# Optimization experiments

Hardware: AMD Instinct MI355X
Metric: run time of the kernel (lower is better)

## Reference

```python
import jax, jax.numpy as jnp
import numpy as np

N = 50000      # nodes
E = 600000     # edges
IN = 128       # input_dim
HID = 128      # hidden_dim
OUT = 128      # output_dim
H = 4          # heads
D = OUT // H   # head dim
R = 4          # rel_num
L = 2          # n_layer
M = 10000      # len(idx)
EPS = 1e-5


def setup_inputs() -> dict:
    key = jax.random.key(0)
    ks = jax.random.split(key, 16)
    f = jax.random.normal
    inp = {
        "x": f(ks[0], (N, IN), jnp.float32),
        "proj_w": f(ks[1], (IN, HID), jnp.float32) / np.sqrt(IN).astype(np.float32),
        "proj_b": jnp.zeros((HID,), jnp.float32),
        "bn_gamma": jnp.ones((HID,), jnp.float32),
        "bn_beta": jnp.zeros((HID,), jnp.float32),
        # per-layer HGTConv params (stacked on leading L axis; layer0 in=HID, layer1 in=OUT, equal here)
        "q_w": f(ks[2], (L, HID, OUT), jnp.float32) / np.sqrt(HID).astype(np.float32),
        "q_b": jnp.zeros((L, OUT), jnp.float32),
        "k_w": f(ks[3], (L, HID, OUT), jnp.float32) / np.sqrt(HID).astype(np.float32),
        "k_b": jnp.zeros((L, OUT), jnp.float32),
        "v_w": f(ks[4], (L, HID, OUT), jnp.float32) / np.sqrt(HID).astype(np.float32),
        "v_b": jnp.zeros((L, OUT), jnp.float32),
        "a_w": f(ks[5], (L, OUT, OUT), jnp.float32) / np.sqrt(OUT).astype(np.float32),
        "a_b": jnp.zeros((L, OUT), jnp.float32),
        "skip": jnp.ones((L,), jnp.float32),
        "a_rel": f(ks[6], (L, R, H, D, D), jnp.float32) / np.sqrt(D).astype(np.float32),
        "m_rel": f(ks[7], (L, R, H, D, D), jnp.float32) / np.sqrt(D).astype(np.float32),
        "p_rel": jnp.ones((L, R, H), jnp.float32),
        "edge_index": jax.random.randint(ks[8], (2, E), 0, N, dtype=jnp.int32),
        "edge_type": jax.random.randint(ks[9], (E,), 0, R, dtype=jnp.int32),
        "idx": jax.random.randint(ks[10], (M,), 0, N, dtype=jnp.int32),
    }
    return inp


def _hgt_forward(x, proj_w, proj_b, bn_gamma, bn_beta, q_w, q_b, k_w, k_b, v_w, v_b,
                 a_w, a_b, skip, a_rel, m_rel, p_rel, edge_index, edge_type, idx):
    # proj + BatchNorm1d (training-mode batch statistics, biased variance)
    h = x @ proj_w + proj_b
    mu = h.mean(axis=0)
    var = jnp.mean((h - mu) ** 2, axis=0)
    h = (h - mu) * jax.lax.rsqrt(var + EPS) * bn_gamma + bn_beta

    src, dst = edge_index[0], edge_index[1]          # message from src(j) to dst(i)
    seg = dst * R + edge_type                        # per-(dst, relation) softmax segments
    scale = np.float32(1.0 / np.sqrt(D))

    for l in range(L):
        q = (h @ q_w[l] + q_b[l]).reshape(N, H, D)
        k = (h @ k_w[l] + k_b[l]).reshape(N, H, D)
        v = (h @ v_w[l] + v_b[l]).reshape(N, H, D)
        # relation-specific key/value transforms for every node/relation: [N,R,H,D]
        k_all = jnp.einsum('nhd,rhde->nrhe', k, a_rel[l])
        v_all = jnp.einsum('nhd,rhde->nrhe', v, m_rel[l])
        k_e = k_all[src, edge_type]                  # [E,H,D]
        v_e = v_all[src, edge_type]                  # [E,H,D]
        score = jnp.sum(q[dst] * k_e, axis=-1) * p_rel[l][edge_type] * scale  # [E,H]
        # per-relation segment softmax over incoming edges of each dst node
        smax = jax.ops.segment_max(score, seg, num_segments=N * R)
        e = jnp.exp(score - smax[seg])
        denom = jax.ops.segment_sum(e, seg, num_segments=N * R)
        alpha = e / denom[seg]                        # [E,H]
        out = jax.ops.segment_sum(alpha[..., None] * v_e, dst, num_segments=N)
        out = out.reshape(N, OUT)
        out = jax.nn.gelu(out, approximate=False) @ a_w[l] + a_b[l]
        b = jax.nn.sigmoid(skip[l])                   # learned skip gate
        h = b * out + (1.0 - b) * h                   # dims match -> residual mix
    return h[idx]


def reference(x, proj_w, proj_b, bn_gamma, bn_beta, q_w, q_b, k_w, k_b, v_w, v_b,
              a_w, a_b, skip, a_rel, m_rel, p_rel, edge_index, edge_type, idx):
    return _hgt_forward(x, proj_w, proj_b, bn_gamma, bn_beta, q_w, q_b, k_w, k_b,
                        v_w, v_b, a_w, a_b, skip, a_rel, m_rel, p_rel,
                        edge_index, edge_type, idx)
```

## Files before the change

kernel.cpp:

```cpp
#include <hip/hip_runtime.h>
#include <math.h>

#define NN 50000
#define EE 600000
#define MOUT 10000
#define DEGCAP 384
#define NT4 (NN * 4)

typedef short bf16x8 __attribute__((ext_vector_type(8)));
typedef float f32x4 __attribute__((ext_vector_type(4)));

__device__ __forceinline__ unsigned short f2bf(float x) {
    unsigned int u = __float_as_uint(x);
    u = (u + 0x7FFFu + ((u >> 16) & 1u)) >> 16;
    return (unsigned short)u;
}
__device__ __forceinline__ float bf2f(unsigned int b) {
    return __uint_as_float(b << 16);
}
__device__ __forceinline__ uint4 pack8bf(float4 a, float4 b) {
    uint4 r;
    r.x = (unsigned int)f2bf(a.x) | ((unsigned int)f2bf(a.y) << 16);
    r.y = (unsigned int)f2bf(a.z) | ((unsigned int)f2bf(a.w) << 16);
    r.z = (unsigned int)f2bf(b.x) | ((unsigned int)f2bf(b.y) << 16);
    r.w = (unsigned int)f2bf(b.z) | ((unsigned int)f2bf(b.w) << 16);
    return r;
}

__global__ __launch_bounds__(256) void prep_kernel(
    const float* __restrict__ proj_w, const float* __restrict__ a_w,
    const float* __restrict__ q_w, const float* __restrict__ q_b,
    const float* __restrict__ a_rel,
    const float* __restrict__ k_w, const float* __restrict__ k_b,
    const float* __restrict__ v_w, const float* __restrict__ v_b,
    const float* __restrict__ m_rel, const float* __restrict__ p_rel,
    unsigned short* __restrict__ wt_pa, unsigned short* __restrict__ qkvw,
    float* __restrict__ fbias, unsigned short* __restrict__ msg_wt,
    int* __restrict__ cnt, float* __restrict__ stats)
{
    const int b = blockIdx.x, t = threadIdx.x;
    if (b < 192) {
        int wi = b >> 6;
        int flat = (b & 63) * 256 + t;
        int n = flat >> 7, c = flat & 127;
        const float* src = (wi == 0) ? proj_w : (wi == 1) ? a_w : a_w + 16384;
        wt_pa[(size_t)wi * 16384 + n * 128 + c] = f2bf(src[c * 128 + n]);
    } else if (b < 960) {
        int q = b - 192;
        int l = q >= 384 ? 1 : 0;
        int flat = (q - l * 384) * 256 + t;
        int nrow = flat >> 7, c = flat & 127;
        unsigned short* wt = qkvw + (size_t)l * 98304;
        float* fb = fbias + l * 768;
        if (nrow < 512) {
            int r = nrow >> 7, hh = (nrow >> 5) & 3, d = nrow & 31;
            float prl = p_rel[l * 16 + r * 4 + hh] * 0.17677669529663687f;
            const float* qwc = q_w + (size_t)l * 16384 + c * 128 + hh * 32;
            const float* ar  = a_rel + (size_t)(l * 4 + r) * 4096 + hh * 1024 + d * 32;
            float s = 0.f;
            #pragma unroll 8
            for (int e = 0; e < 32; ++e) s += qwc[e] * ar[e];
            wt[(size_t)nrow * 128 + c] = f2bf(s * prl);
            if (c == 0) {
                const float* qb = q_b + l * 128 + hh * 32;
                float bb = 0.f;
                #pragma unroll 8
                for (int e = 0; e < 32; ++e) bb += qb[e] * ar[e];
                fb[nrow] = bb * prl;
            }
        } else {
            int j = nrow - 512;
            int tt = j >> 3, s = j & 7;
            int col = 4 * tt + (s & 3);
            const float* w  = (s < 4) ? k_w : v_w;
            const float* bb = (s < 4) ? k_b : v_b;
            wt[(size_t)nrow * 128 + c] = f2bf(w[(size_t)l * 16384 + c * 128 + col]);
            if (c == 0) fb[nrow] = bb[l * 128 + col];
        }
    } else if (b < 1088) {
        int q = b - 960;
        int l = q >= 64 ? 1 : 0;
        int flat = (q - l * 64) * 256 + t;
        int r = flat >> 12, rem = flat & 4095;
        int n = rem >> 5, d = rem & 31;
        float val = m_rel[(size_t)(l * 4 + r) * 4096 + (n >> 5) * 1024 + d * 32 + (n & 31)];
        msg_wt[(size_t)l * 16384 + r * 4096 + n * 32 + d] = f2bf(val);
    } else {
        int i = (b - 1088) * 256 + t;
        if (i < NT4) cnt[i] = 0;
        if (i < 256) stats[i] = 0.f;
    }
}

__global__ __launch_bounds__(256) void hist_kernel(const int* __restrict__ ei,
    const int* __restrict__ et, int* __restrict__ cnt, int E)
{
    int e = blockIdx.x * 256 + threadIdx.x;
    if (e < E) atomicAdd(&cnt[ei[E + e] * 4 + et[e]], 1);
}

__global__ __launch_bounds__(256) void scan_block_kernel(const int* __restrict__ cnt,
    int* __restrict__ excl, int* __restrict__ bsum, int n)
{
    __shared__ int tmp[256];
    int i = blockIdx.x * 256 + threadIdx.x;
    int v = (i < n) ? cnt[i] : 0;
    tmp[threadIdx.x] = v;
    __syncthreads();
    for (int ofs = 1; ofs < 256; ofs <<= 1) {
        int t = (threadIdx.x >= ofs) ? tmp[threadIdx.x - ofs] : 0;
        __syncthreads();
        tmp[threadIdx.x] += t;
        __syncthreads();
    }
    if (i < n) excl[i] = tmp[threadIdx.x] - v;
    if (threadIdx.x == 255) bsum[blockIdx.x] = tmp[255];
}

__global__ __launch_bounds__(256) void scan_add_kernel(int* __restrict__ excl,
    const int* __restrict__ bsum, int* __restrict__ fill,
    int* __restrict__ maskz, int n, int total)
{
    __shared__ int red[256];
    const int b = blockIdx.x;
    int partial = 0;
    for (int j = threadIdx.x; j < b; j += 256) partial += bsum[j];
    red[threadIdx.x] = partial;
    __syncthreads();
    for (int ofs = 128; ofs > 0; ofs >>= 1) {
        if (threadIdx.x < ofs) red[threadIdx.x] += red[threadIdx.x + ofs];
        __syncthreads();
    }
    int prefix = red[0];
    int i = b * 256 + threadIdx.x;
    if (i < n) {
        int o = excl[i] + prefix;
        excl[i] = o;
        fill[i] = o;
    }
    if (i < 12500) maskz[i] = 0;
    if (b == 0 && threadIdx.x == 0) excl[n] = total;
}

__global__ __launch_bounds__(256) void scatter_kernel(const int* __restrict__ ei,
    const int* __restrict__ et, int* __restrict__ fill, int* __restrict__ pack,
    const int* __restrict__ idxp, unsigned char* __restrict__ mask, int Mo, int E)
{
    int e = blockIdx.x * 256 + threadIdx.x;
    if (e >= E) return;
    int seg = ei[E + e] * 4 + et[e];
    int p = atomicAdd(&fill[seg], 1);
    pack[p] = ei[e];
    if (e < Mo) mask[idxp[e]] = 1;
}

__global__ __launch_bounds__(256) void projstats_kernel(
    const float* __restrict__ X, const unsigned short* __restrict__ Wt,
    const float* __restrict__ bias, unsigned short* __restrict__ Cb,
    float* __restrict__ stats, int M)
{
    __shared__ unsigned short As[128 * 40];
    __shared__ unsigned short Bs[128 * 40];
    const int t = threadIdx.x;
    const int wave = t >> 6, lane = t & 63;
    const int quad = lane >> 4, l16 = lane & 15;
    const int row0 = blockIdx.x * 128;
    const int wr = (wave & 1) * 64, wc = (wave >> 1) * 64;
    const int sr = t >> 1, sc = (t & 1) * 16;
    const int grow = row0 + sr;

    f32x4 acc[4][4];
    #pragma unroll
    for (int i = 0; i < 4; ++i)
        #pragma unroll
        for (int j = 0; j < 4; ++j)
            acc[i][j] = (f32x4){0.f, 0.f, 0.f, 0.f};

    uint4 av0 = make_uint4(0,0,0,0), av1 = av0, bv0, bv1;
    if (grow < M) {
        const float4* ap = (const float4*)(X + (size_t)grow * 128 + sc);
        av0 = pack8bf(ap[0], ap[1]);
        av1 = pack8bf(ap[2], ap[3]);
    }
    {
        const uint4* bp = (const uint4*)(Wt + (size_t)sr * 128 + sc);
        bv0 = bp[0]; bv1 = bp[1];
    }
    for (int it = 0; it < 4; ++it) {
        __syncthreads();
        *(uint4*)(As + sr * 40 + sc)     = av0;
        *(uint4*)(As + sr * 40 + sc + 8) = av1;
        *(uint4*)(Bs + sr * 40 + sc)     = bv0;
        *(uint4*)(Bs + sr * 40 + sc + 8) = bv1;
        __syncthreads();
        if (it + 1 < 4) {
            int kb = (it + 1) * 32;
            if (grow < M) {
                const float4* ap = (const float4*)(X + (size_t)grow * 128 + kb + sc);
                av0 = pack8bf(ap[0], ap[1]);
                av1 = pack8bf(ap[2], ap[3]);
            }
            const uint4* bp = (const uint4*)(Wt + (size_t)sr * 128 + kb + sc);
            bv0 = bp[0]; bv1 = bp[1];
        }
        bf16x8 af[4], bfr[4];
        #pragma unroll
        for (int f = 0; f < 4; ++f) {
            af[f]  = *(const bf16x8*)(As + (wr + f * 16 + l16) * 40 + quad * 8);
            bfr[f] = *(const bf16x8*)(Bs + (wc + f * 16 + l16) * 40 + quad * 8);
        }
        #pragma unroll
        for (int fr = 0; fr < 4; ++fr)
            #pragma unroll
            for (int fc = 0; fc < 4; ++fc)
                acc[fr][fc] = __builtin_amdgcn_mfma_f32_16x16x32_bf16(
                    af[fr], bfr[fc], acc[fr][fc], 0, 0, 0);
    }

    #pragma unroll
    for (int fc = 0; fc < 4; ++fc) {
        const int col = wc + fc * 16 + l16;
        const float bv = bias[col];
        float s = 0.f, s2 = 0.f;
        #pragma unroll
        for (int fr = 0; fr < 4; ++fr)
            #pragma unroll
            for (int reg = 0; reg < 4; ++reg) {
                int row = row0 + wr + fr * 16 + quad * 4 + reg;
                float val = acc[fr][fc][reg] + bv;
                if (row < M) {
                    Cb[(size_t)row * 128 + col] = f2bf(val);
                    s += val; s2 += val * val;
                }
            }
        s  += __shfl_xor(s, 16);  s  += __shfl_xor(s, 32);
        s2 += __shfl_xor(s2, 16); s2 += __shfl_xor(s2, 32);
        if (quad == 0) {
            atomicAdd(&stats[col], s);
            atomicAdd(&stats[128 + col], s2);
        }
    }
}

__global__ __launch_bounds__(256) void bnqkv_kernel(
    const unsigned short* __restrict__ hb, const float* __restrict__ stats,
    const float* __restrict__ gamma, const float* __restrict__ beta,
    const unsigned short* __restrict__ qkvw, const float* __restrict__ fbias,
    unsigned short* __restrict__ hn, unsigned short* __restrict__ qkv, int M)
{
    __shared__ unsigned short hS[128 * 136];
    __shared__ unsigned short Bs[128 * 40];
    __shared__ float mulS[128], addS[128];
    const int t = threadIdx.x;
    const int row0 = blockIdx.x * 128;
    const int ch0 = blockIdx.y * 2;
    if (t < 128) {
        float invN = 1.f / 50000.f;
        float mu = stats[t] * invN;
        float var = stats[128 + t] * invN - mu * mu;
        float ml = rsqrtf(var + 1e-5f) * gamma[t];
        mulS[t] = ml;
        addS[t] = beta[t] - mu * ml;
    }
    __syncthreads();
    #pragma unroll
    for (int u = 0; u < 8; ++u) {
        int li = t + u * 256;
        int row = li >> 4, c0 = (li & 15) * 8;
        uint4 pk = make_uint4(0, 0, 0, 0);
        if (row0 + row < M)
            pk = ((const uint4*)(hb + (size_t)(row0 + row) * 128))[li & 15];
        unsigned int w[4] = {pk.x, pk.y, pk.z, pk.w};
        uint4 o;
        unsigned int ov[4];
        #pragma unroll
        for (int g = 0; g < 4; ++g) {
            int c = c0 + g * 2;
            float a0 = bf2f(w[g] & 0xFFFFu) * mulS[c]     + addS[c];
            float a1 = bf2f(w[g] >> 16)     * mulS[c + 1] + addS[c + 1];
            ov[g] = (unsigned int)f2bf(a0) | ((unsigned int)f2bf(a1) << 16);
        }
        o.x = ov[0]; o.y = ov[1]; o.z = ov[2]; o.w = ov[3];
        *(uint4*)(hS + row * 136 + c0) = o;
        if (blockIdx.y == 0 && row0 + row < M)
            ((uint4*)(hn + (size_t)(row0 + row) * 128))[li & 15] = o;
    }
    __syncthreads();

    const int wave = t >> 6, lane = t & 63;
    const int quad = lane >> 4, l16 = lane & 15;
    const int wr = (wave & 1) * 64, wcl = (wave >> 1) * 64;
    const int sr = t >> 1, scc = (t & 1) * 16;

    uint4 pv0, pv1;
    {
        const uint4* bp = (const uint4*)(qkvw + (size_t)(ch0 * 128 + sr) * 128 + scc);
        pv0 = bp[0]; pv1 = bp[1];
    }
    for (int ch = ch0; ch < ch0 + 2; ++ch) {
        f32x4 acc[4][4];
        #pragma unroll
        for (int i = 0; i < 4; ++i)
            #pragma unroll
            for (int j = 0; j < 4; ++j)
                acc[i][j] = (f32x4){0.f, 0.f, 0.f, 0.f};
        for (int it = 0; it < 4; ++it) {
            __syncthreads();
            *(uint4*)(Bs + sr * 40 + scc)     = pv0;
            *(uint4*)(Bs + sr * 40 + scc + 8) = pv1;
            __syncthreads();
            int nit = it + 1, nch = ch;
            if (nit == 4) { nit = 0; ++nch; }
            if (nch < ch0 + 2) {
                const uint4* bp = (const uint4*)(qkvw + (size_t)(nch * 128 + sr) * 128 + nit * 32 + scc);
                pv0 = bp[0]; pv1 = bp[1];
            }
            bf16x8 af[4], bfr[4];
            #pragma unroll
            for (int f = 0; f < 4; ++f) {
                af[f]  = *(const bf16x8*)(hS + (wr + f * 16 + l16) * 136 + it * 32 + quad * 8);
                bfr[f] = *(const bf16x8*)(Bs + (wcl + f * 16 + l16) * 40 + quad * 8);
            }
            #pragma unroll
            for (int fr = 0; fr < 4; ++fr)
                #pragma unroll
                for (int fc = 0; fc < 4; ++fc)
                    acc[fr][fc] = __builtin_amdgcn_mfma_f32_16x16x32_bf16(
                        af[fr], bfr[fc], acc[fr][fc], 0, 0, 0);
        }
        float b4[4];
        #pragma unroll
        for (int fc = 0; fc < 4; ++fc)
            b4[fc] = fbias[ch * 128 + wcl + fc * 16 + l16];
        #pragma unroll
        for (int fr = 0; fr < 4; ++fr)
            #pragma unroll
            for (int reg = 0; reg < 4; ++reg) {
                int row = row0 + wr + fr * 16 + quad * 4 + reg;
                if (row >= M) continue;
                #pragma unroll
                for (int fc = 0; fc < 4; ++fc) {
                    int col = ch * 128 + wcl + fc * 16 + l16;
                    qkv[(size_t)row * 768 + col] = f2bf(acc[fr][fc][reg] + b4[fc]);
                }
            }
    }
}

__global__ __launch_bounds__(256) void agg_fused_kernel(
    const unsigned short* __restrict__ qkv,
    const unsigned short* __restrict__ qbuf, int qpitch,
    const int* __restrict__ off4, const int* __restrict__ pack,
    const int* __restrict__ rowmap, unsigned short* __restrict__ aggb, int count)
{
    __shared__ int spack[4][DEGCAP];
    const int wv = threadIdx.x >> 6;
    const int lane = threadIdx.x & 63;
    const int l32 = lane & 31;
    const int hi = lane >> 5;
    const int unit = blockIdx.x * 4 + wv;
    if (unit >= count) return;
    const int node = rowmap ? __builtin_amdgcn_readfirstlane(rowmap[unit]) : unit;

    const uint2* qrow = (const uint2*)(qbuf + (size_t)unit * qpitch);
    uint2 quv[4];
    #pragma unroll
    for (int r = 0; r < 4; ++r) quv[r] = qrow[r * 32 + l32];

    int off_r[5];
    #pragma unroll
    for (int i = 0; i < 5; ++i)
        off_r[i] = __builtin_amdgcn_readfirstlane(off4[node * 4 + i]);
    const int beg = off_r[0];
    const int deg = off_r[4] - beg;
    const bool cached = deg <= DEGCAP;

    if (cached) {
        for (int i = lane; i < deg; i += 64) spack[wv][i] = pack[beg + i];
        asm volatile("s_waitcnt vmcnt(0) lgkmcnt(0)" ::: "memory");
    }

    uint2 outw[4];
    #pragma unroll
    for (int r = 0; r < 4; ++r) {
        float q0 = bf2f(quv[r].x & 0xFFFFu), q1 = bf2f(quv[r].x >> 16);
        float q2 = bf2f(quv[r].y & 0xFFFFu), q3 = bf2f(quv[r].y >> 16);
        float den = 0.f, a0 = 0.f, a1 = 0.f, a2 = 0.f, a3 = 0.f;

        if (cached) {
            const int rb = off_r[r] - beg, re = off_r[r + 1] - beg;
            for (int i = rb; i < re; i += 4) {
                int i0 = i + hi;      if (i0 >= re) i0 = re - 1;
                int i1 = i + 2 + hi;  if (i1 >= re) i1 = re - 1;
                int s0 = spack[wv][i0], s1 = spack[wv][i1];
                uint4 kv0 = *(const uint4*)(qkv + (size_t)s0 * 768 + 512 + l32 * 8);
                uint4 kv1 = *(const uint4*)(qkv + (size_t)s1 * 768 + 512 + l32 * 8);
                {
                    float p = q0 * bf2f(kv0.x & 0xFFFFu) + q1 * bf2f(kv0.x >> 16)
                            + q2 * bf2f(kv0.y & 0xFFFFu) + q3 * bf2f(kv0.y >> 16);
                    p += __shfl_xor(p, 1); p += __shfl_xor(p, 2); p += __shfl_xor(p, 4);
                    float e = __expf(fminf(fmaxf(p, -80.f), 80.f));
                    if (i + hi >= re) e = 0.f;
                    den += e;
                    a0 += e * bf2f(kv0.z & 0xFFFFu); a1 += e * bf2f(kv0.z >> 16);
                    a2 += e * bf2f(kv0.w & 0xFFFFu); a3 += e * bf2f(kv0.w >> 16);
                }
                {
                    float p = q0 * bf2f(kv1.x & 0xFFFFu) + q1 * bf2f(kv1.x >> 16)
                            + q2 * bf2f(kv1.y & 0xFFFFu) + q3 * bf2f(kv1.y >> 16);
                    p += __shfl_xor(p, 1); p += __shfl_xor(p, 2); p += __shfl_xor(p, 4);
                    float e = __expf(fminf(fmaxf(p, -80.f), 80.f));
                    if (i + 2 + hi >= re) e = 0.f;
                    den += e;
                    a0 += e * bf2f(kv1.z & 0xFFFFu); a1 += e * bf2f(kv1.z >> 16);
                    a2 += e * bf2f(kv1.w & 0xFFFFu); a3 += e * bf2f(kv1.w >> 16);
                }
            }
        } else {
            const int pe_end = off_r[r + 1];
            for (int pp = off_r[r]; pp < pe_end; pp += 2) {
                int pe = pp + hi; if (pe >= pe_end) pe = pe_end - 1;
                int src = pack[pe];
                uint4 kv = *(const uint4*)(qkv + (size_t)src * 768 + 512 + l32 * 8);
                float p = q0 * bf2f(kv.x & 0xFFFFu) + q1 * bf2f(kv.x >> 16)
                        + q2 * bf2f(kv.y & 0xFFFFu) + q3 * bf2f(kv.y >> 16);
                p += __shfl_xor(p, 1); p += __shfl_xor(p, 2); p += __shfl_xor(p, 4);
                float e = __expf(fminf(fmaxf(p, -80.f), 80.f));
                if (pp + hi >= pe_end) e = 0.f;
                den += e;
                a0 += e * bf2f(kv.z & 0xFFFFu); a1 += e * bf2f(kv.z >> 16);
                a2 += e * bf2f(kv.w & 0xFFFFu); a3 += e * bf2f(kv.w >> 16);
            }
        }
        den += __shfl_xor(den, 32);
        a0  += __shfl_xor(a0, 32);
        a1  += __shfl_xor(a1, 32);
        a2  += __shfl_xor(a2, 32);
        a3  += __shfl_xor(a3, 32);
        float inv = den > 0.f ? 1.f / den : 0.f;
        outw[r].x = (unsigned int)f2bf(a0 * inv) | ((unsigned int)f2bf(a1 * inv) << 16);
        outw[r].y = (unsigned int)f2bf(a2 * inv) | ((unsigned int)f2bf(a3 * inv) << 16);
    }
    if (hi == 0) {
        uint2* op = (uint2*)(aggb + (size_t)unit * 512);
        #pragma unroll
        for (int r = 0; r < 4; ++r) op[r * 32 + l32] = outw[r];
    }
}

__global__ __launch_bounds__(256) void mlpqkv_kernel(
    const unsigned short* __restrict__ A, const unsigned short* __restrict__ W3c,
    const unsigned short* __restrict__ AWt, const float* __restrict__ a_bias,
    const float* __restrict__ skipv, const unsigned short* __restrict__ hres,
    const unsigned short* __restrict__ qkvw1, const float* __restrict__ fbias1,
    const unsigned char* __restrict__ mask,
    unsigned short* __restrict__ h1, unsigned short* __restrict__ qkv, int M)
{
    __shared__ unsigned short Bs[128 * 40];
    __shared__ unsigned short msgS[64 * 136];
    const int t = threadIdx.x;
    const int wave = t >> 6, lane = t & 63;
    const int quad = lane >> 4, l16 = lane & 15;
    const int row0 = blockIdx.x * 64;
    const int wcl = wave * 32;
    const int sr = t >> 1, scc = (t & 1) * 16;
    const int sr4 = t >> 2, sc4 = (t & 3) * 32;
    const int grow = row0 + sr4;
    const bool rvalid = grow < M;

    f32x4 acc[4][2];
    #pragma unroll
    for (int i = 0; i < 4; ++i)
        #pragma unroll
        for (int j = 0; j < 2; ++j)
            acc[i][j] = (f32x4){0.f, 0.f, 0.f, 0.f};

    uint4 av[4];
    #pragma unroll
    for (int j = 0; j < 4; ++j) av[j] = make_uint4(0, 0, 0, 0);
    if (rvalid) {
        const uint4* ap = (const uint4*)(A + (size_t)grow * 512 + sc4);
        #pragma unroll
        for (int j = 0; j < 4; ++j) av[j] = ap[j];
    }
    uint4 bw0, bw1;
    {
        const uint4* bp = (const uint4*)(W3c + sr * 32 + scc);
        bw0 = bp[0]; bw1 = bp[1];
    }
    for (int it = 0; it < 4; ++it) {
        __syncthreads();
        #pragma unroll
        for (int j = 0; j < 4; ++j)
            *(uint4*)(msgS + sr4 * 136 + sc4 + j * 8) = av[j];
        *(uint4*)(Bs + sr * 40 + scc)     = bw0;
        *(uint4*)(Bs + sr * 40 + scc + 8) = bw1;
        __syncthreads();
        if (it + 1 < 4) {
            if (rvalid) {
                const uint4* ap = (const uint4*)(A + (size_t)grow * 512 + (it + 1) * 128 + sc4);
                #pragma unroll
                for (int j = 0; j < 4; ++j) av[j] = ap[j];
            }
            const uint4* bp = (const uint4*)(W3c + (it + 1) * 4096 + sr * 32 + scc);
            bw0 = bp[0]; bw1 = bp[1];
        }
        bf16x8 af[4], bfr[2];
        #pragma unroll
        for (int f = 0; f < 4; ++f)
            af[f] = *(const bf16x8*)(msgS + (f * 16 + l16) * 136 + wave * 32 + quad * 8);
        #pragma unroll
        for (int f = 0; f < 2; ++f)
            bfr[f] = *(const bf16x8*)(Bs + (wcl + f * 16 + l16) * 40 + quad * 8);
        #pragma unroll
        for (int fr = 0; fr < 4; ++fr)
            #pragma unroll
            for (int fc = 0; fc < 2; ++fc)
                acc[fr][fc] = __builtin_amdgcn_mfma_f32_16x16x32_bf16(
                    af[fr], bfr[fc], acc[fr][fc], 0, 0, 0);
    }
    __syncthreads();

    #pragma unroll
    for (int fr = 0; fr < 4; ++fr)
        #pragma unroll
        for (int reg = 0; reg < 4; ++reg) {
            int rl = fr * 16 + quad * 4 + reg;
            #pragma unroll
            for (int fc = 0; fc < 2; ++fc) {
                int col = wcl + fc * 16 + l16;
                float v = acc[fr][fc][reg];
                float gl = 0.5f * v * (1.f + erff(v * 0.70710678118654752f));
                msgS[rl * 136 + col] = f2bf(gl);
            }
        }

    f32x4 acc2[4][2];
    #pragma unroll
    for (int i = 0; i < 4; ++i)
        #pragma unroll
        for (int j = 0; j < 2; ++j)
            acc2[i][j] = (f32x4){0.f, 0.f, 0.f, 0.f};
    uint4 pv0, pv1;
    {
        const uint4* bp = (const uint4*)(AWt + (size_t)sr * 128 + scc);
        pv0 = bp[0]; pv1 = bp[1];
    }
    for (int it = 0; it < 4; ++it) {
        __syncthreads();
        *(uint4*)(Bs + sr * 40 + scc)     = pv0;
        *(uint4*)(Bs + sr * 40 + scc + 8) = pv1;
        __syncthreads();
        if (it + 1 < 4) {
            const uint4* bp = (const uint4*)(AWt + (size_t)sr * 128 + (it + 1) * 32 + scc);
            pv0 = bp[0]; pv1 = bp[1];
        } else {
            const uint4* bp = (const uint4*)(qkvw1 + (size_t)(4 * 128 + sr) * 128 + scc);
            pv0 = bp[0]; pv1 = bp[1];
        }
        bf16x8 af[4], bfr[2];
        #pragma unroll
        for (int f = 0; f < 4; ++f)
            af[f] = *(const bf16x8*)(msgS + (f * 16 + l16) * 136 + it * 32 + quad * 8);
        #pragma unroll
        for (int f = 0; f < 2; ++f)
            bfr[f] = *(const bf16x8*)(Bs + (wcl + f * 16 + l16) * 40 + quad * 8);
        #pragma unroll
        for (int fr = 0; fr < 4; ++fr)
            #pragma unroll
            for (int fc = 0; fc < 2; ++fc)
                acc2[fr][fc] = __builtin_amdgcn_mfma_f32_16x16x32_bf16(
                    af[fr], bfr[fc], acc2[fr][fc], 0, 0, 0);
    }

    const float gate = 1.f / (1.f + __expf(-skipv[0]));
    __syncthreads();
    #pragma unroll
    for (int fr = 0; fr < 4; ++fr)
        #pragma unroll
        for (int reg = 0; reg < 4; ++reg) {
            int rl = fr * 16 + quad * 4 + reg;
            int row = row0 + rl;
            const bool rv = row < M;
            const bool mw = rv && mask[row];
            #pragma unroll
            for (int fc = 0; fc < 2; ++fc) {
                int col = wcl + fc * 16 + l16;
                float val = acc2[fr][fc][reg] + a_bias[col];
                float nv = val;
                if (rv) {
                    unsigned int hu = hres[(size_t)row * 128 + col];
                    nv = gate * val + (1.f - gate) * bf2f(hu);
                    if (mw) h1[(size_t)row * 128 + col] = f2bf(nv);
                }
                msgS[rl * 136 + col] = f2bf(nv);
            }
        }

    for (int ch = 4; ch < 6; ++ch) {
        f32x4 acc3[4][2];
        #pragma unroll
        for (int i = 0; i < 4; ++i)
            #pragma unroll
            for (int j = 0; j < 2; ++j)
                acc3[i][j] = (f32x4){0.f, 0.f, 0.f, 0.f};
        for (int it = 0; it < 4; ++it) {
            __syncthreads();
            *(uint4*)(Bs + sr * 40 + scc)     = pv0;
            *(uint4*)(Bs + sr * 40 + scc + 8) = pv1;
            __syncthreads();
            int nit = it + 1, nch = ch;
            if (nit == 4) { nit = 0; ++nch; }
            if (nch < 6) {
                const uint4* bp = (const uint4*)(qkvw1 + (size_t)(nch * 128 + sr) * 128 + nit * 32 + scc);
                pv0 = bp[0]; pv1 = bp[1];
            }
            bf16x8 af[4], bfr[2];
            #pragma unroll
            for (int f = 0; f < 4; ++f)
                af[f] = *(const bf16x8*)(msgS + (f * 16 + l16) * 136 + it * 32 + quad * 8);
            #pragma unroll
            for (int f = 0; f < 2; ++f)
                bfr[f] = *(const bf16x8*)(Bs + (wcl + f * 16 + l16) * 40 + quad * 8);
            #pragma unroll
            for (int fr = 0; fr < 4; ++fr)
                #pragma unroll
                for (int fc = 0; fc < 2; ++fc)
                    acc3[fr][fc] = __builtin_amdgcn_mfma_f32_16x16x32_bf16(
                        af[fr], bfr[fc], acc3[fr][fc], 0, 0, 0);
        }
        float b2[2];
        #pragma unroll
        for (int fc = 0; fc < 2; ++fc)
            b2[fc] = fbias1[ch * 128 + wcl + fc * 16 + l16];
        #pragma unroll
        for (int fr = 0; fr < 4; ++fr)
            #pragma unroll
            for (int reg = 0; reg < 4; ++reg) {
                int row = row0 + fr * 16 + quad * 4 + reg;
                if (row >= M) continue;
                #pragma unroll
                for (int fc = 0; fc < 2; ++fc) {
                    int col = ch * 128 + wcl + fc * 16 + l16;
                    qkv[(size_t)row * 768 + col] = f2bf(acc3[fr][fc][reg] + b2[fc]);
                }
            }
    }
}

__global__ __launch_bounds__(256) void q1_kernel(
    const unsigned short* __restrict__ h1, const int* __restrict__ idxp,
    const unsigned short* __restrict__ qkvw1, const float* __restrict__ fbias1,
    unsigned short* __restrict__ q1, int M)
{
    __shared__ unsigned short hS[128 * 136];
    __shared__ unsigned short Bs[128 * 40];
    const int t = threadIdx.x;
    const int row0 = blockIdx.x * 128;
    const int ch = blockIdx.y;
    #pragma unroll
    for (int u = 0; u < 8; ++u) {
        int li = t + u * 256;
        int row = li >> 4, c = li & 15;
        uint4 pk = make_uint4(0, 0, 0, 0);
        if (row0 + row < M) {
            int node = idxp[row0 + row];
            pk = ((const uint4*)(h1 + (size_t)node * 128))[c];
        }
        *(uint4*)(hS + row * 136 + c * 8) = pk;
    }
    __syncthreads();

    const int wave = t >> 6, lane = t & 63;
    const int quad = lane >> 4, l16 = lane & 15;
    const int wr = (wave & 1) * 64, wcl = (wave >> 1) * 64;
    const int sr = t >> 1, scc = (t & 1) * 16;
    uint4 pv0, pv1;
    {
        const uint4* bp = (const uint4*)(qkvw1 + (size_t)(ch * 128 + sr) * 128 + scc);
        pv0 = bp[0]; pv1 = bp[1];
    }
    f32x4 acc[4][4];
    #pragma unroll
    for (int i = 0; i < 4; ++i)
        #pragma unroll
        for (int j = 0; j < 4; ++j)
            acc[i][j] = (f32x4){0.f, 0.f, 0.f, 0.f};
    for (int it = 0; it < 4; ++it) {
        __syncthreads();
        *(uint4*)(Bs + sr * 40 + scc)     = pv0;
        *(uint4*)(Bs + sr * 40 + scc + 8) = pv1;
        __syncthreads();
        if (it + 1 < 4) {
            const uint4* bp = (const uint4*)(qkvw1 + (size_t)(ch * 128 + sr) * 128 + (it + 1) * 32 + scc);
            pv0 = bp[0]; pv1 = bp[1];
        }
        bf16x8 af[4], bfr[4];
        #pragma unroll
        for (int f = 0; f < 4; ++f) {
            af[f]  = *(const bf16x8*)(hS + (wr + f * 16 + l16) * 136 + it * 32 + quad * 8);
            bfr[f] = *(const bf16x8*)(Bs + (wcl + f * 16 + l16) * 40 + quad * 8);
        }
        #pragma unroll
        for (int fr = 0; fr < 4; ++fr)
            #pragma unroll
            for (int fc = 0; fc < 4; ++fc)
                acc[fr][fc] = __builtin_amdgcn_mfma_f32_16x16x32_bf16(
                    af[fr], bfr[fc], acc[fr][fc], 0, 0, 0);
    }
    float b4[4];
    #pragma unroll
    for (int fc = 0; fc < 4; ++fc)
        b4[fc] = fbias1[ch * 128 + wcl + fc * 16 + l16];
    #pragma unroll
    for (int fr = 0; fr < 4; ++fr)
        #pragma unroll
        for (int reg = 0; reg < 4; ++reg) {
            int row = row0 + wr + fr * 16 + quad * 4 + reg;
            if (row >= M) continue;
            #pragma unroll
            for (int fc = 0; fc < 4; ++fc) {
                int col = ch * 128 + wcl + fc * 16 + l16;
                q1[(size_t)row * 512 + col] = f2bf(acc[fr][fc][reg] + b4[fc]);
            }
        }
}

__global__ __launch_bounds__(256) void mlp1_kernel(
    const unsigned short* __restrict__ A, const unsigned short* __restrict__ W3c,
    const unsigned short* __restrict__ AWt, const float* __restrict__ a_bias,
    const float* __restrict__ skipv, const unsigned short* __restrict__ hres,
    const int* __restrict__ rowmap, float* __restrict__ out, int M)
{
    __shared__ unsigned short Bs[128 * 40];
    __shared__ unsigned short msgS[64 * 136];
    const int t = threadIdx.x;
    const int wave = t >> 6, lane = t & 63;
    const int quad = lane >> 4, l16 = lane & 15;
    const int row0 = blockIdx.x * 64;
    const int wcl = wave * 32;
    const int sr = t >> 1, scc = (t & 1) * 16;
    const int sr4 = t >> 2, sc4 = (t & 3) * 32;
    const int grow = row0 + sr4;
    const bool rvalid = grow < M;

    f32x4 acc[4][2];
    #pragma unroll
    for (int i = 0; i < 4; ++i)
        #pragma unroll
        for (int j = 0; j < 2; ++j)
            acc[i][j] = (f32x4){0.f, 0.f, 0.f, 0.f};

    uint4 av[4];
    #pragma unroll
    for (int j = 0; j < 4; ++j) av[j] = make_uint4(0, 0, 0, 0);
    if (rvalid) {
        const uint4* ap = (const uint4*)(A + (size_t)grow * 512 + sc4);
        #pragma unroll
        for (int j = 0; j < 4; ++j) av[j] = ap[j];
    }
    uint4 bw0, bw1;
    {
        const uint4* bp = (const uint4*)(W3c + sr * 32 + scc);
        bw0 = bp[0]; bw1 = bp[1];
    }
    for (int it = 0; it < 4; ++it) {
        __syncthreads();
        #pragma unroll
        for (int j = 0; j < 4; ++j)
            *(uint4*)(msgS + sr4 * 136 + sc4 + j * 8) = av[j];
        *(uint4*)(Bs + sr * 40 + scc)     = bw0;
        *(uint4*)(Bs + sr * 40 + scc + 8) = bw1;
        __syncthreads();
        if (it + 1 < 4) {
            if (rvalid) {
                const uint4* ap = (const uint4*)(A + (size_t)grow * 512 + (it + 1) * 128 + sc4);
                #pragma unroll
                for (int j = 0; j < 4; ++j) av[j] = ap[j];
            }
            const uint4* bp = (const uint4*)(W3c + (it + 1) * 4096 + sr * 32 + scc);
            bw0 = bp[0]; bw1 = bp[1];
        }
        bf16x8 af[4], bfr[2];
        #pragma unroll
        for (int f = 0; f < 4; ++f)
            af[f] = *(const bf16x8*)(msgS + (f * 16 + l16) * 136 + wave * 32 + quad * 8);
        #pragma unroll
        for (int f = 0; f < 2; ++f)
            bfr[f] = *(const bf16x8*)(Bs + (wcl + f * 16 + l16) * 40 + quad * 8);
        #pragma unroll
        for (int fr = 0; fr < 4; ++fr)
            #pragma unroll
            for (int fc = 0; fc < 2; ++fc)
                acc[fr][fc] = __builtin_amdgcn_mfma_f32_16x16x32_bf16(
                    af[fr], bfr[fc], acc[fr][fc], 0, 0, 0);
    }
    __syncthreads();

    #pragma unroll
    for (int fr = 0; fr < 4; ++fr)
        #pragma unroll
        for (int reg = 0; reg < 4; ++reg) {
            int rl = fr * 16 + quad * 4 + reg;
            #pragma unroll
            for (int fc = 0; fc < 2; ++fc) {
                int col = wcl + fc * 16 + l16;
                float v = acc[fr][fc][reg];
                float gl = 0.5f * v * (1.f + erff(v * 0.70710678118654752f));
                msgS[rl * 136 + col] = f2bf(gl);
            }
        }

    f32x4 acc2[4][2];
    #pragma unroll
    for (int i = 0; i < 4; ++i)
        #pragma unroll
        for (int j = 0; j < 2; ++j)
            acc2[i][j] = (f32x4){0.f, 0.f, 0.f, 0.f};
    uint4 pv0, pv1;
    {
        const uint4* bp = (const uint4*)(AWt + (size_t)sr * 128 + scc);
        pv0 = bp[0]; pv1 = bp[1];
    }
    for (int it = 0; it < 4; ++it) {
        __syncthreads();
        *(uint4*)(Bs + sr * 40 + scc)     = pv0;
        *(uint4*)(Bs + sr * 40 + scc + 8) = pv1;
        __syncthreads();
        if (it + 1 < 4) {
            const uint4* bp = (const uint4*)(AWt + (size_t)sr * 128 + (it + 1) * 32 + scc);
            pv0 = bp[0]; pv1 = bp[1];
        }
        bf16x8 af[4], bfr[2];
        #pragma unroll
        for (int f = 0; f < 4; ++f)
            af[f] = *(const bf16x8*)(msgS + (f * 16 + l16) * 136 + it * 32 + quad * 8);
        #pragma unroll
        for (int f = 0; f < 2; ++f)
            bfr[f] = *(const bf16x8*)(Bs + (wcl + f * 16 + l16) * 40 + quad * 8);
        #pragma unroll
        for (int fr = 0; fr < 4; ++fr)
            #pragma unroll
            for (int fc = 0; fc < 2; ++fc)
                acc2[fr][fc] = __builtin_amdgcn_mfma_f32_16x16x32_bf16(
                    af[fr], bfr[fc], acc2[fr][fc], 0, 0, 0);
    }

    const float gate = 1.f / (1.f + __expf(-skipv[0]));
    #pragma unroll
    for (int fr = 0; fr < 4; ++fr)
        #pragma unroll
        for (int reg = 0; reg < 4; ++reg) {
            int row = row0 + fr * 16 + quad * 4 + reg;
            if (row >= M) continue;
            int hrow = rowmap[row];
            #pragma unroll
            for (int fc = 0; fc < 2; ++fc) {
                int col = wcl + fc * 16 + l16;
                float val = acc2[fr][fc][reg] + a_bias[col];
                float nv = gate * val + (1.f - gate) * bf2f((unsigned int)hres[(size_t)hrow * 128 + col]);
                out[(size_t)row * 128 + col] = nv;
            }
        }
}

extern "C" void kernel_launch(void* const* d_in, const int* in_sizes, int n_in,
                              void* d_out, int out_size, void* d_ws, size_t ws_size,
                              hipStream_t stream)
{
    const float* x      = (const float*)d_in[0];
    const float* proj_w = (const float*)d_in[1];
    const float* proj_b = (const float*)d_in[2];
    const float* bn_g   = (const float*)d_in[3];
    const float* bn_b   = (const float*)d_in[4];
    const float* q_w    = (const float*)d_in[5];
    const float* q_b    = (const float*)d_in[6];
    const float* k_w    = (const float*)d_in[7];
    const float* k_b    = (const float*)d_in[8];
    const float* v_w    = (const float*)d_in[9];
    const float* v_b    = (const float*)d_in[10];
    const float* a_w    = (const float*)d_in[11];
    const float* a_b    = (const float*)d_in[12];
    const float* skip   = (const float*)d_in[13];
    const float* a_rel  = (const float*)d_in[14];
    const float* m_rel  = (const float*)d_in[15];
    const float* p_rel  = (const float*)d_in[16];
    const int* edge_index = (const int*)d_in[17];
    const int* edge_type  = (const int*)d_in[18];
    const int* idx        = (const int*)d_in[19];
    float* out = (float*)d_out;

    const int N = NN, E = EE;
    float* ws = (float*)d_ws;
    size_t o = 0;
    float* stats  = ws + o;  o += 256;
    float* fbias  = ws + o;  o += 2 * 768;
    int* cnt  = (int*)(ws + o); o += NT4;
    int* off4 = (int*)(ws + o); o += NT4 + 1;
    int* fill = (int*)(ws + o); o += NT4;
    int* bsum = (int*)(ws + o); o += 1024;
    int* pack = (int*)(ws + o); o += E;
    unsigned short* x_bf   = (unsigned short*)(ws + o); o += (size_t)N * 64;
    unsigned short* h_bf   = (unsigned short*)(ws + o); o += (size_t)N * 64;
    unsigned short* hn_bf  = (unsigned short*)(ws + o); o += (size_t)N * 64;
    unsigned short* h1_bf  = (unsigned short*)(ws + o); o += (size_t)N * 64;
    unsigned short* qkv_bf = (unsigned short*)(ws + o); o += (size_t)N * 384;
    unsigned short* agg_bf = (unsigned short*)(ws + o); o += (size_t)N * 256;
    unsigned short* wt_pa  = (unsigned short*)(ws + o); o += 3 * 16384 / 2;
    unsigned short* qkvw   = (unsigned short*)(ws + o); o += 2 * 98304 / 2;
    unsigned short* msg_wt = (unsigned short*)(ws + o); o += 2 * 65536 / 2;

    unsigned char* mask = (unsigned char*)cnt;
    unsigned short* q1 = x_bf;

    const int NB4 = (NT4 + 255) / 256;
    const int g = (N + 127) / 128;

    prep_kernel<<<1088 + NB4, 256, 0, stream>>>(
        proj_w, a_w, q_w, q_b, a_rel, k_w, k_b, v_w, v_b, m_rel, p_rel,
        wt_pa, qkvw, fbias, msg_wt, cnt, stats);

    hist_kernel<<<(E + 255) / 256, 256, 0, stream>>>(edge_index, edge_type, cnt, E);
    scan_block_kernel<<<NB4, 256, 0, stream>>>(cnt, off4, bsum, NT4);
    scan_add_kernel<<<NB4, 256, 0, stream>>>(off4, bsum, fill, cnt, NT4, E);
    scatter_kernel<<<(E + 255) / 256, 256, 0, stream>>>(edge_index, edge_type, fill,
                                                        pack, idx, mask, MOUT, E);

    projstats_kernel<<<g, 256, 0, stream>>>(x, wt_pa, proj_b, h_bf, stats, N);

    {
        dim3 grid(g, 3);
        bnqkv_kernel<<<grid, 256, 0, stream>>>(h_bf, stats, bn_g, bn_b, qkvw, fbias,
                                               hn_bf, qkv_bf, N);
    }

    agg_fused_kernel<<<(N + 3) / 4, 256, 0, stream>>>(qkv_bf, qkv_bf, 768,
                                                      off4, pack, nullptr, agg_bf, N);

    mlpqkv_kernel<<<(N + 63) / 64, 256, 0, stream>>>(agg_bf, msg_wt, wt_pa + 16384, a_b, skip,
                                                     hn_bf, qkvw + 98304, fbias + 768,
                                                     mask, h1_bf, qkv_bf, N);

    {
        dim3 gq((MOUT + 127) / 128, 4);
        q1_kernel<<<gq, 256, 0, stream>>>(h1_bf, idx, qkvw + 98304, fbias + 768, q1, MOUT);
    }

    agg_fused_kernel<<<(MOUT + 3) / 4, 256, 0, stream>>>(qkv_bf, q1, 512,
                                                         off4, pack, idx, agg_bf, MOUT);

    mlp1_kernel<<<(MOUT + 63) / 64, 256, 0, stream>>>(agg_bf, msg_wt + 16384,
                                                      wt_pa + 2 * 16384, a_b + 128,
                                                      skip + 1, h1_bf, idx, out, MOUT);
}
```

Measured before the change: 402.7 us.

## Fuse histogram into prep and edge scatter into projection kernel launch

Moves the zeroing of the count and stats buffers to memset calls and runs the edge histogram inside the prep kernel's extra blocks. The edge scatter now runs as extra blocks of the projection+stats GEMM launch. The projection GEMM itself is retiled to 64-row blocks, with the whole A tile staged in shared memory once. The aim is fewer kernel launches and better SM fill, but the histogram now races only with independent prep work, and the mixed-role blocks may imbalance scheduling.

New measurement: 391.0 us. 1.03x faster.

```diff
diff --git a/kernel.cpp b/kernel.cpp
--- a/kernel.cpp
+++ b/kernel.cpp
@@ -34,9 +34,10 @@
     const float* __restrict__ k_w, const float* __restrict__ k_b,
     const float* __restrict__ v_w, const float* __restrict__ v_b,
     const float* __restrict__ m_rel, const float* __restrict__ p_rel,
+    const int* __restrict__ ei, const int* __restrict__ et,
     unsigned short* __restrict__ wt_pa, unsigned short* __restrict__ qkvw,
     float* __restrict__ fbias, unsigned short* __restrict__ msg_wt,
-    int* __restrict__ cnt, float* __restrict__ stats)
+    int* __restrict__ cnt, int E)
 {
     const int b = blockIdx.x, t = threadIdx.x;
     if (b < 192) {
@@ -86,17 +87,9 @@
         float val = m_rel[(size_t)(l * 4 + r) * 4096 + (n >> 5) * 1024 + d * 32 + (n & 31)];
         msg_wt[(size_t)l * 16384 + r * 4096 + n * 32 + d] = f2bf(val);
     } else {
-        int i = (b - 1088) * 256 + t;
-        if (i < NT4) cnt[i] = 0;
-        if (i < 256) stats[i] = 0.f;
-    }
-}
-
-__global__ __launch_bounds__(256) void hist_kernel(const int* __restrict__ ei,
-    const int* __restrict__ et, int* __restrict__ cnt, int E)
-{
-    int e = blockIdx.x * 256 + threadIdx.x;
-    if (e < E) atomicAdd(&cnt[ei[E + e] * 4 + et[e]], 1);
+        int e = (b - 1088) * 256 + t;
+        if (e < E) atomicAdd(&cnt[ei[E + e] * 4 + et[e]], 1);
+    }
 }
 
 __global__ __launch_bounds__(256) void scan_block_kernel(const int* __restrict__ cnt,
@@ -142,91 +135,96 @@
     if (b == 0 && threadIdx.x == 0) excl[n] = total;
 }
 
-__global__ __launch_bounds__(256) void scatter_kernel(const int* __restrict__ ei,
-    const int* __restrict__ et, int* __restrict__ fill, int* __restrict__ pack,
-    const int* __restrict__ idxp, unsigned char* __restrict__ mask, int Mo, int E)
-{
-    int e = blockIdx.x * 256 + threadIdx.x;
-    if (e >= E) return;
-    int seg = ei[E + e] * 4 + et[e];
-    int p = atomicAdd(&fill[seg], 1);
-    pack[p] = ei[e];
-    if (e < Mo) mask[idxp[e]] = 1;
-}
-
 __global__ __launch_bounds__(256) void projstats_kernel(
     const float* __restrict__ X, const unsigned short* __restrict__ Wt,
     const float* __restrict__ bias, unsigned short* __restrict__ Cb,
-    float* __restrict__ stats, int M)
+    float* __restrict__ stats, int M,
+    const int* __restrict__ ei, const int* __restrict__ et,
+    int* __restrict__ fill, int* __restrict__ pack,
+    const int* __restrict__ idxp, unsigned char* __restrict__ mask,
+    int Mo, int E, int psB)
 {
-    __shared__ unsigned short As[128 * 40];
+    __shared__ unsigned short As[64 * 136];
     __shared__ unsigned short Bs[128 * 40];
     const int t = threadIdx.x;
+    if (blockIdx.x >= psB) {
+        int e = (blockIdx.x - psB) * 256 + t;
+        if (e < E) {
+            int seg = ei[E + e] * 4 + et[e];
+            int p = atomicAdd(&fill[seg], 1);
+            pack[p] = ei[e];
+            if (e < Mo) mask[idxp[e]] = 1;
+        }
+        return;
+    }
     const int wave = t >> 6, lane = t & 63;
     const int quad = lane >> 4, l16 = lane & 15;
-    const int row0 = blockIdx.x * 128;
-    const int wr = (wave & 1) * 64, wc = (wave >> 1) * 64;
-    const int sr = t >> 1, sc = (t & 1) * 16;
-    const int grow = row0 + sr;
-
-    f32x4 acc[4][4];
+    const int row0 = blockIdx.x * 64;
+    const int wcl = wave * 32;
+    const int sr = t >> 1, scc = (t & 1) * 16;
+    const int sr4 = t >> 2, sc4 = (t & 3) * 32;
+    const int grow = row0 + sr4;
+    const bool rvalid = grow < M;
+
+    f32x4 acc[4][2];
     #pragma unroll
     for (int i = 0; i < 4; ++i)
         #pragma unroll
-        for (int j = 0; j < 4; ++j)
+        for (int j = 0; j < 2; ++j)
             acc[i][j] = (f32x4){0.f, 0.f, 0.f, 0.f};
 
-    uint4 av0 = make_uint4(0,0,0,0), av1 = av0, bv0, bv1;
-    if (grow < M) {
-        const float4* ap = (const float4*)(X + (size_t)grow * 128 + sc);
-        av0 = pack8bf(ap[0], ap[1]);
-        av1 = pack8bf(ap[2], ap[3]);
-    }
+    uint4 av[4];
+    #pragma unroll
+    for (int j = 0; j < 4; ++j) av[j] = make_uint4(0, 0, 0, 0);
+    if (rvalid) {
+        const float4* ap = (const float4*)(X + (size_t)grow * 128 + sc4);
+        #pragma unroll
+        for (int j = 0; j < 4; ++j) av[j] = pack8bf(ap[2 * j], ap[2 * j + 1]);
+    }
+    uint4 pv0, pv1;
     {
-        const uint4* bp = (const uint4*)(Wt + (size_t)sr * 128 + sc);
-        bv0 = bp[0]; bv1 = bp[1];
+        const uint4* bp = (const uint4*)(Wt + (size_t)sr * 128 + scc);
+        pv0 = bp[0]; pv1 = bp[1];
     }
     for (int it = 0; it < 4; ++it) {
         __syncthreads();
-        *(uint4*)(As + sr * 40 + sc)     = av0;
-        *(uint4*)(As + sr * 40 + sc + 8) = av1;
-        *(uint4*)(Bs + sr * 40 + sc)     = bv0;
-        *(uint4*)(Bs + sr * 40 + sc + 8) = bv1;
+        if (it == 0) {
+            #pragma unroll
+            for (int j = 0; j < 4; ++j)
+                *(uint4*)(As + sr4 * 136 + sc4 + j * 8) = av[j];
+        }
+        *(uint4*)(Bs + sr * 40 + scc)     = pv0;
+        *(uint4*)(Bs + sr * 40 + scc + 8) = pv1;
         __syncthreads();
         if (it + 1 < 4) {
-            int kb = (it + 1) * 32;
-            if (grow < M) {
-                const float4* ap = (const float4*)(X + (size_t)grow * 128 + kb + sc);
-                av0 = pack8bf(ap[0], ap[1]);
-                av1 = pack8bf(ap[2], ap[3]);
-            }
-            const uint4* bp = (const uint4*)(Wt + (size_t)sr * 128 + kb + sc);
-            bv0 = bp[0]; bv1 = bp[1];
-        }
-        bf16x8 af[4], bfr[4];
-        #pragma unroll
-        for (int f = 0; f < 4; ++f) {
-            af[f]  = *(const bf16x8*)(As + (wr + f * 16 + l16) * 40 + quad * 8);
-            bfr[f] = *(const bf16x8*)(Bs + (wc + f * 16 + l16) * 40 + quad * 8);
-        }
+            const uint4* bp = (const uint4*)(Wt + (size_t)sr * 128 + (it + 1) * 32 + scc);
+            pv0 = bp[0]; pv1 = bp[1];
+        }
+        bf16x8 af[4], bfr[2];
+        #pragma unroll
+        for (int f = 0; f < 4; ++f)
+            af[f] = *(const bf16x8*)(As + (f * 16 + l16) * 136 + it * 32 + quad * 8);
+        #pragma unroll
+        for (int f = 0; f < 2; ++f)
+            bfr[f] = *(const bf16x8*)(Bs + (wcl + f * 16 + l16) * 40 + quad * 8);
         #pragma unroll
         for (int fr = 0; fr < 4; ++fr)
             #pragma unroll
-            for (int fc = 0; fc < 4; ++fc)
+            for (int fc = 0; fc < 2; ++fc)
                 acc[fr][fc] = __builtin_amdgcn_mfma_f32_16x16x32_bf16(
                     af[fr], bfr[fc], acc[fr][fc], 0, 0, 0);
     }
 
     #pragma unroll
-    for (int fc = 0; fc < 4; ++fc) {
-        const int col = wc + fc * 16 + l16;
+    for (int fc = 0; fc < 2; ++fc) {
+        const int col = wcl + fc * 16 + l16;
         const float bv = bias[col];
         float s = 0.f, s2 = 0.f;
         #pragma unroll
         for (int fr = 0; fr < 4; ++fr)
             #pragma unroll
             for (int reg = 0; reg < 4; ++reg) {
-                int row = row0 + wr + fr * 16 + quad * 4 + reg;
+                int row = row0 + fr * 16 + quad * 4 + reg;
                 float val = acc[fr][fc][reg] + bv;
                 if (row < M) {
                     Cb[(size_t)row * 128 + col] = f2bf(val);
@@ -914,22 +912,26 @@
     unsigned short* q1 = x_bf;
 
     const int NB4 = (NT4 + 255) / 256;
-    const int g = (N + 127) / 128;
-
-    prep_kernel<<<1088 + NB4, 256, 0, stream>>>(
+    const int EB  = (E + 255) / 256;
+    const int PSB = (N + 63) / 64;
+
+    hipMemsetAsync(stats, 0, 256 * sizeof(float), stream);
+    hipMemsetAsync(cnt, 0, (size_t)NT4 * sizeof(int), stream);
+
+    prep_kernel<<<1088 + EB, 256, 0, stream>>>(
         proj_w, a_w, q_w, q_b, a_rel, k_w, k_b, v_w, v_b, m_rel, p_rel,
-        wt_pa, qkvw, fbias, msg_wt, cnt, stats);
-
-    hist_kernel<<<(E + 255) / 256, 256, 0, stream>>>(edge_index, edge_type, cnt, E);
+        edge_index, edge_type,
+        wt_pa, qkvw, fbias, msg_wt, cnt, E);
+
     scan_block_kernel<<<NB4, 256, 0, stream>>>(cnt, off4, bsum, NT4);
     scan_add_kernel<<<NB4, 256, 0, stream>>>(off4, bsum, fill, cnt, NT4, E);
-    scatter_kernel<<<(E + 255) / 256, 256, 0, stream>>>(edge_index, edge_type, fill,
-                                                        pack, idx, mask, MOUT, E);
-
-    projstats_kernel<<<g, 256, 0, stream>>>(x, wt_pa, proj_b, h_bf, stats, N);
+
+    projstats_kernel<<<PSB + EB, 256, 0, stream>>>(x, wt_pa, proj_b, h_bf, stats, N,
+                                                   edge_index, edge_type, fill, pack,
+                                                   idx, mask, MOUT, E, PSB);
 
     {
-        dim3 grid(g, 3);
+        dim3 grid((N + 127) / 128, 3);
         bnqkv_kernel<<<grid, 256, 0, stream>>>(h_bf, stats, bn_g, bn_b, qkvw, fbias,
                                                hn_bf, qkv_bf, N);
     }
```
